# Performance work log

Hardware: AMD Instinct MI355X
Metric: run time of the kernel (lower is better)

## Reference

```python
import jax, jax.numpy as jnp
import numpy as np

B, N, D, H, O = 8, 2048, 64, 64, 64
ALPHA = 2.0  # LeakyReLU negative slope per module default
NEG = -9e15


def _lin(x, W, b):
    # torch nn.Linear: y = x @ W.T + b, W is [out, in]
    return x @ W.T + b


def setup_inputs() -> dict:
    key = jax.random.key(0)
    ks = jax.random.split(key, 32)
    f32 = jnp.float32
    x = jax.random.normal(ks[0], (B, N, D), f32)
    adj = jax.random.randint(ks[1], (B, N, N), 0, 2).astype(f32)
    c = jax.random.normal(ks[2], (B, N, H), f32)
    h = jax.random.normal(ks[3], (B, N, H), f32)
    s = 0.1
    W = jax.random.normal(ks[4], (D, H), f32) * s           # GAT weight
    a = jax.random.normal(ks[5], (2 * H, 1), f32) * s       # GAT attention vector
    def lin(k, out_d, in_d):
        k1, k2 = jax.random.split(k)
        return (jax.random.normal(k1, (out_d, in_d), f32) * s,
                jax.random.normal(k2, (out_d,), f32) * s)
    Wf, bWf = lin(ks[6], H, H); Wi, bWi = lin(ks[7], H, H)
    Wo, bWo = lin(ks[8], H, H); Wc, bWc = lin(ks[9], H, H)
    Uf, bUf = lin(ks[10], H, D); Ui, bUi = lin(ks[11], H, D)
    Uo, bUo = lin(ks[12], H, D); Uc, bUc = lin(ks[13], H, D)
    Wout, bout = lin(ks[14], O, 2 * H)
    return dict(x=x, adj=adj, c=c, h=h, W=W, a=a,
                Wf=Wf, bWf=bWf, Wi=Wi, bWi=bWi, Wo=Wo, bWo=bWo, Wc=Wc, bWc=bWc,
                Uf=Uf, bUf=bUf, Ui=Ui, bUi=bUi, Uo=Uo, bUo=bUo, Uc=Uc, bUc=bUc,
                Wout=Wout, bout=bout)


def reference(x, adj, c, h, W, a,
              Wf, bWf, Wi, bWi, Wo, bWo, Wc, bWc,
              Uf, bUf, Ui, bUi, Uo, bUo, Uc, bUc,
              Wout, bout):
    # ---- GraphAttentionLayer (eval mode: dropout is identity) ----
    Wh = x @ W                                   # [B,N,H]
    # e[b,i,j] = leakyrelu(a[:H].Wh_i + a[H:].Wh_j) -- same math as the
    a_src = (Wh @ a[:H]).squeeze(-1)             # [B,N]
    a_dst = (Wh @ a[H:]).squeeze(-1)             # [B,N]
    e = jax.nn.leaky_relu(a_src[:, :, None] + a_dst[:, None, :], ALPHA)  # [B,N,N]
    att = jnp.where(adj > 0, e, NEG)
    att = jax.nn.softmax(att, axis=2)
    x_hidden = jax.nn.elu(att @ Wh)              # [B,N,H] (concat=True)
    # ---- LSTMLayer step ----
    f_t = jax.nn.sigmoid(_lin(h, Wf, bWf) + _lin(x, Uf, bUf))
    i_t = jax.nn.sigmoid(_lin(h, Wi, bWi) + _lin(x, Ui, bUi))
    o_t = jax.nn.sigmoid(_lin(h, Wo, bWo) + _lin(x, Uo, bUo))
    c_hat = jnp.tanh(_lin(h, Wc, bWc) + _lin(x, Uc, bUc))
    c_t = f_t * c + i_t * c_hat
    h_t = o_t * jax.nn.relu(c_t)                 # gate = nn.ReLU() default
    total = jnp.concatenate([x_hidden, h_t], axis=2)  # [B,N,2H]
    output = jax.nn.relu(_lin(total, Wout, bout))     # [B,N,O]
    return (output, h_t, c_t)
```

## Files before the change

### kernel.cpp

```cpp
#include <hip/hip_runtime.h>
#include <math.h>

#define B_ 8
#define N_ 2048
#define NT_ (B_*N_)
#define OUTSZ (NT_*64)

#define WS_ASRC  0
#define WS_ADST  (WS_ASRC + NT_)
#define WS_EJ    (WS_ADST + NT_)
#define WS_C1    (WS_EJ + NT_)
#define WS_C2    (WS_C1 + NT_)
#define WS_THR   (WS_C2 + NT_)
#define WS_GMAX  (WS_THR + NT_)
#define WS_WT    (WS_GMAX + 32)
#define WS_BB    (WS_WT + 128*256)
#define WS_WOT   (WS_BB + 256)
#define WS_PD    (WS_WOT + 128*64)
#define WS_PN    (WS_PD + 4*NT_)

typedef float f32x4 __attribute__((ext_vector_type(4)));
typedef __bf16 bf16x8 __attribute__((ext_vector_type(8)));
typedef __bf16 bf16x4 __attribute__((ext_vector_type(4)));

__device__ __forceinline__ float lrelu2(float x) { return x > 0.f ? x : 2.f * x; }
__device__ __forceinline__ float f4get(const float4& v, int k) { return k==0?v.x:(k==1?v.y:(k==2?v.z:v.w)); }

__global__ __launch_bounds__(256) void k1_wh(const float* __restrict__ x, const float* __restrict__ W,
                                             const float* __restrict__ a, float* __restrict__ ws,
                                             __bf16* __restrict__ whT,
                                             const float* Wf, const float* Wi, const float* Wo, const float* Wc,
                                             const float* Uf, const float* Ui, const float* Uo, const float* Uc,
                                             const float* bWf, const float* bWi, const float* bWo, const float* bWc,
                                             const float* bUf, const float* bUi, const float* bUo, const float* bUc,
                                             const float* Wout)
{
    __shared__ float xl[64 * 68];
    __shared__ float Wl[64 * 68];
    int t = threadIdx.x;
    if (blockIdx.x >= 256) {
        int idx = (blockIdx.x - 256) * 256 + t;
        if (idx < 128 * 256) {
            int k = idx >> 8, o = idx & 255;
            int g = o >> 6, u = o & 63;
            const float* Wg = (g == 0) ? Wf : (g == 1) ? Wi : (g == 2) ? Wo : Wc;
            const float* Ug = (g == 0) ? Uf : (g == 1) ? Ui : (g == 2) ? Uo : Uc;
            ws[WS_WT + idx] = (k < 64) ? Wg[u * 64 + k] : Ug[u * 64 + (k - 64)];
        } else if (idx < 128 * 256 + 256) {
            int o = idx - 128 * 256;
            int g = o >> 6, u = o & 63;
            const float* bW = (g == 0) ? bWf : (g == 1) ? bWi : (g == 2) ? bWo : bWc;
            const float* bU = (g == 0) ? bUf : (g == 1) ? bUi : (g == 2) ? bUo : bUc;
            ws[WS_BB + o] = bW[u] + bU[u];
        } else if (idx < 128 * 256 + 256 + 128 * 64) {
            int j = idx - (128 * 256 + 256);
            int k = j >> 6, u = j & 63;
            ws[WS_WOT + j] = Wout[u * 128 + k];
        }
        return;
    }
    int i0 = blockIdx.x * 64;
    #pragma unroll
    for (int it = 0; it < 4; ++it) {
        int f = t + 256 * it;
        int r = f >> 4, q = f & 15;
        *(float4*)&xl[r * 68 + q * 4] = *(const float4*)&x[i0 * 64 + f * 4];
        *(float4*)&Wl[r * 68 + q * 4] = *(const float4*)&W[f * 4];
    }
    __syncthreads();
    int cg = t & 15, rg = t >> 4;
    int c0 = cg * 4, r0 = rg * 4;
    float acc[4][4] = {};
    #pragma unroll
    for (int d0 = 0; d0 < 64; d0 += 4) {
        float4 wv[4], xv[4];
        #pragma unroll
        for (int k = 0; k < 4; ++k) wv[k] = *(float4*)&Wl[(d0 + k) * 68 + c0];
        #pragma unroll
        for (int ri = 0; ri < 4; ++ri) xv[ri] = *(float4*)&xl[(r0 + ri) * 68 + d0];
        #pragma unroll
        for (int ri = 0; ri < 4; ++ri)
            #pragma unroll
            for (int k = 0; k < 4; ++k) {
                float xs = f4get(xv[ri], k);
                acc[ri][0] += xs * wv[k].x; acc[ri][1] += xs * wv[k].y;
                acc[ri][2] += xs * wv[k].z; acc[ri][3] += xs * wv[k].w;
            }
    }
    int b = i0 >> 11;
    int rowb0 = (i0 & 2047) + r0;
    #pragma unroll
    for (int cj = 0; cj < 4; ++cj) {
        bf16x4 v;
        v[0] = (__bf16)acc[0][cj]; v[1] = (__bf16)acc[1][cj];
        v[2] = (__bf16)acc[2][cj]; v[3] = (__bf16)acc[3][cj];
        *(bf16x4*)&whT[((size_t)(b * 64 + c0 + cj)) * N_ + rowb0] = v;
    }
    float4 a0 = *(const float4*)&a[c0];
    float4 a1 = *(const float4*)&a[64 + c0];
    #pragma unroll
    for (int ri = 0; ri < 4; ++ri) {
        int row = i0 + r0 + ri;
        float s0 = acc[ri][0]*a0.x + acc[ri][1]*a0.y + acc[ri][2]*a0.z + acc[ri][3]*a0.w;
        float s1 = acc[ri][0]*a1.x + acc[ri][1]*a1.y + acc[ri][2]*a1.z + acc[ri][3]*a1.w;
        #pragma unroll
        for (int m = 1; m < 16; m <<= 1) { s0 += __shfl_xor(s0, m, 64); s1 += __shfl_xor(s1, m, 64); }
        if (cg == 0) { ws[WS_ASRC + row] = s0; ws[WS_ADST + row] = s1; }
    }
}

__global__ __launch_bounds__(256) void k1b_prep(float* ws)
{
    __shared__ float red[256];
    __shared__ float gsh;
    int b = blockIdx.x, t = threadIdx.x;
    float m = -3.0e38f;
    for (int j = t; j < N_; j += 256) {
        float v = ws[WS_ADST + b * N_ + j];
        ws[WS_EJ + b * N_ + j] = __expf(v);
        m = fmaxf(m, v);
    }
    red[t] = m; __syncthreads();
    for (int s = 128; s > 0; s >>= 1) { if (t < s) red[t] = fmaxf(red[t], red[t + s]); __syncthreads(); }
    if (t == 0) { gsh = red[0]; ws[WS_GMAX + b] = red[0]; }
    __syncthreads();
    float gmax = gsh;
    for (int i = t; i < N_; i += 256) {
        float as = ws[WS_ASRC + b * N_ + i];
        float M = lrelu2(as + gmax);
        ws[WS_C1 + b * N_ + i]  = __expf(as - M);
        ws[WS_C2 + b * N_ + i]  = __expf(2.f * as - M);
        ws[WS_THR + b * N_ + i] = __expf(-as);
    }
}

__global__ __launch_bounds__(512, 4) void k2v4(const float* __restrict__ adj,
                                               const __bf16* __restrict__ whT,
                                               float* __restrict__ ws)
{
    __shared__ float lsa[2][8][16][68];
    __shared__ float lsd[2][8][16];
    int tid = threadIdx.x;
    int lane = tid & 63, w = tid >> 6;
    int r = lane & 15, g = lane >> 4;
    int jr = blockIdx.x & 3;
    int rslab = blockIdx.x >> 2;
    int b = rslab >> 4;
    int row_base = rslab * 128;
    int jbeg = jr * 512 + w * 64;

    bf16x8 bfr[2][4];
    #pragma unroll
    for (int ks = 0; ks < 2; ++ks)
        #pragma unroll
        for (int n = 0; n < 4; ++n)
            bfr[ks][n] = *(const bf16x8*)&whT[(size_t)(b * 64 + n * 16 + r) * N_ + jbeg + ks * 32 + g * 8];
    float ejr[2][8];
    #pragma unroll
    for (int ks = 0; ks < 2; ++ks) {
        float4 e0 = *(const float4*)&ws[WS_EJ + b * N_ + jbeg + ks * 32 + g * 8];
        float4 e1 = *(const float4*)&ws[WS_EJ + b * N_ + jbeg + ks * 32 + g * 8 + 4];
        ejr[ks][0]=e0.x; ejr[ks][1]=e0.y; ejr[ks][2]=e0.z; ejr[ks][3]=e0.w;
        ejr[ks][4]=e1.x; ejr[ks][5]=e1.y; ejr[ks][6]=e1.z; ejr[ks][7]=e1.w;
    }

    float4 av[3][4];
    float c1v[3], c2v[3], thv[3];

#define LDT(T, S)                                                                  \
    {                                                                              \
        int row0_ = row_base + (T) * 16;                                           \
        const float* ap_ = &adj[(size_t)(row0_ + r) * N_ + jbeg];                  \
        av[S][0] = *(const float4*)&ap_[g * 8];                                    \
        av[S][1] = *(const float4*)&ap_[g * 8 + 4];                                \
        av[S][2] = *(const float4*)&ap_[32 + g * 8];                               \
        av[S][3] = *(const float4*)&ap_[32 + g * 8 + 4];                           \
        c1v[S] = ws[WS_C1 + row0_ + r];                                            \
        c2v[S] = ws[WS_C2 + row0_ + r];                                            \
        thv[S] = ws[WS_THR + row0_ + r];                                           \
    }

    LDT(0, 0);
    LDT(1, 1);

    #pragma unroll
    for (int t = 0; t < 8; ++t) {
        const int s = t % 3;
        if (t + 2 < 8) { LDT(t + 2, (t + 2) % 3); }
        f32x4 acc[4] = {{0.f,0.f,0.f,0.f},{0.f,0.f,0.f,0.f},{0.f,0.f,0.f,0.f},{0.f,0.f,0.f,0.f}};
        float dsum = 0.f;
        float c1 = c1v[s], c2 = c2v[s], thr = thv[s];
        #pragma unroll
        for (int ks = 0; ks < 2; ++ks) {
            bf16x8 af;
            float ds_ = 0.f;
            #pragma unroll
            for (int e = 0; e < 8; ++e) {
                float avv = f4get(e < 4 ? av[s][ks * 2] : av[s][ks * 2 + 1], e & 3);
                float E = ejr[ks][e];
                float p = (E > thr) ? c1 * E : (c2 * E) * E;
                p = (avv > 0.f) ? p : 0.f;
                ds_ += p;
                af[e] = (__bf16)p;
            }
            dsum += ds_;
            #pragma unroll
            for (int n = 0; n < 4; ++n)
                acc[n] = __builtin_amdgcn_mfma_f32_16x16x32_bf16(af, bfr[ks][n], acc[n], 0, 0, 0);
        }
        dsum += __shfl_xor(dsum, 16, 64);
        dsum += __shfl_xor(dsum, 32, 64);
        #pragma unroll
        for (int n = 0; n < 4; ++n)
            #pragma unroll
            for (int i = 0; i < 4; ++i)
                lsa[t & 1][w][g * 4 + i][n * 16 + r] = acc[n][i];
        if (g == 0) lsd[t & 1][w][r] = dsum;
        asm volatile("s_waitcnt lgkmcnt(0)" ::: "memory");
        __builtin_amdgcn_s_barrier();
        asm volatile("" ::: "memory");
        if (tid < 256) {
            int rl = tid >> 4, h0 = (tid & 15) * 4;
            float4 sv = make_float4(0.f, 0.f, 0.f, 0.f);
            #pragma unroll
            for (int w2 = 0; w2 < 8; ++w2) {
                float4 q = *(const float4*)&lsa[t & 1][w2][rl][h0];
                sv.x += q.x; sv.y += q.y; sv.z += q.z; sv.w += q.w;
            }
            int row0 = row_base + t * 16;
            *(float4*)&ws[WS_PN + ((size_t)jr * NT_ + row0 + rl) * 64 + h0] = sv;
            if (tid < 16) {
                float d = 0.f;
                #pragma unroll
                for (int w2 = 0; w2 < 8; ++w2) d += lsd[t & 1][w2][tid];
                ws[WS_PD + jr * NT_ + row0 + tid] = d;
            }
        }
    }
#undef LDT
}

__global__ __launch_bounds__(256) void k3_lstm(const float* __restrict__ x, const float* __restrict__ c,
                                               const float* __restrict__ h, const float* __restrict__ ws,
                                               float* __restrict__ out)
{
    __shared__ float Al[16 * 132];
    __shared__ float gl[16 * 260];
    int t = threadIdx.x;
    int base = blockIdx.x * 16;
    {
        int r = t >> 4, k0 = (t & 15) * 8;
        const float* src = (k0 < 64) ? &h[(base + r) * 64 + k0] : &x[(base + r) * 64 + (k0 - 64)];
        *(float4*)&Al[r * 132 + k0]     = *(const float4*)&src[0];
        *(float4*)&Al[r * 132 + k0 + 4] = *(const float4*)&src[4];
    }
    __syncthreads();
    int og = t & 63, rg = t >> 6;
    int o0 = og * 4;
    const float* WT = &ws[WS_WT];
    float acc[4][4] = {};
    #pragma unroll
    for (int k0 = 0; k0 < 128; k0 += 4) {
        float4 wv[4], av[4];
        #pragma unroll
        for (int kk = 0; kk < 4; ++kk) wv[kk] = *(const float4*)&WT[(k0 + kk) * 256 + o0];
        #pragma unroll
        for (int rr = 0; rr < 4; ++rr) av[rr] = *(float4*)&Al[(rg + 4 * rr) * 132 + k0];
        #pragma unroll
        for (int rr = 0; rr < 4; ++rr)
            #pragma unroll
            for (int kk = 0; kk < 4; ++kk) {
                float as = f4get(av[rr], kk);
                acc[rr][0] += as * wv[kk].x; acc[rr][1] += as * wv[kk].y;
                acc[rr][2] += as * wv[kk].z; acc[rr][3] += as * wv[kk].w;
            }
    }
    float4 bbv = *(const float4*)&ws[WS_BB + o0];
    #pragma unroll
    for (int rr = 0; rr < 4; ++rr) {
        int r = rg + 4 * rr;
        *(float4*)&gl[r * 260 + o0] = make_float4(acc[rr][0] + bbv.x, acc[rr][1] + bbv.y,
                                                  acc[rr][2] + bbv.z, acc[rr][3] + bbv.w);
    }
    __syncthreads();
    int u = t & 63, rq = t >> 6;
    #pragma unroll
    for (int pp = 0; pp < 4; ++pp) {
        int r = rq + 4 * pp;
        float gf = gl[r * 260 + u];
        float gi = gl[r * 260 + 64 + u];
        float go = gl[r * 260 + 128 + u];
        float gc = gl[r * 260 + 192 + u];
        float fg = 1.f / (1.f + __expf(-gf));
        float ig = 1.f / (1.f + __expf(-gi));
        float oo = 1.f / (1.f + __expf(-go));
        float ch = tanhf(gc);
        float cv = c[(base + r) * 64 + u];
        float ct = fg * cv + ig * ch;
        float ht = oo * fmaxf(ct, 0.f);
        out[OUTSZ + (base + r) * 64 + u] = ht;
        out[2 * OUTSZ + (base + r) * 64 + u] = ct;
    }
}

__global__ __launch_bounds__(256) void k5_out(const float* __restrict__ ws, const float* __restrict__ bout,
                                              float* __restrict__ out)
{
    __shared__ float Al[64 * 132];
    int t = threadIdx.x;
    int base = blockIdx.x * 64;
    const float* ht = &out[OUTSZ];
    #pragma unroll
    for (int it = 0; it < 8; ++it) {
        int f = t + 256 * it;
        int r = f >> 5, q = f & 31;
        int k0 = q * 4;
        int row = base + r;
        float4 v;
        if (k0 < 64) {
            float4 s = make_float4(0.f, 0.f, 0.f, 0.f);
            float d = 0.f;
            #pragma unroll
            for (int jr = 0; jr < 4; ++jr) {
                float4 p = *(const float4*)&ws[WS_PN + ((size_t)jr * NT_ + row) * 64 + k0];
                s.x += p.x; s.y += p.y; s.z += p.z; s.w += p.w;
                d += ws[WS_PD + jr * NT_ + row];
            }
            float inv = 1.f / d;
            v.x = s.x * inv; v.x = v.x > 0.f ? v.x : expm1f(v.x);
            v.y = s.y * inv; v.y = v.y > 0.f ? v.y : expm1f(v.y);
            v.z = s.z * inv; v.z = v.z > 0.f ? v.z : expm1f(v.z);
            v.w = s.w * inv; v.w = v.w > 0.f ? v.w : expm1f(v.w);
        } else {
            v = *(const float4*)&ht[(size_t)row * 64 + (k0 - 64)];
        }
        *(float4*)&Al[r * 132 + k0] = v;
    }
    __syncthreads();
    int cg = t & 15, rgG = t >> 4;
    int c0 = cg * 4, r0 = rgG * 4;
    const float* WT = &ws[WS_WOT];
    float acc[4][4] = {};
    #pragma unroll
    for (int k0 = 0; k0 < 128; k0 += 4) {
        float4 wv[4], av[4];
        #pragma unroll
        for (int kk = 0; kk < 4; ++kk) wv[kk] = *(const float4*)&WT[(k0 + kk) * 64 + c0];
        #pragma unroll
        for (int ri = 0; ri < 4; ++ri) av[ri] = *(float4*)&Al[(r0 + ri) * 132 + k0];
        #pragma unroll
        for (int ri = 0; ri < 4; ++ri)
            #pragma unroll
            for (int kk = 0; kk < 4; ++kk) {
                float as = f4get(av[ri], kk);
                acc[ri][0] += as * wv[kk].x; acc[ri][1] += as * wv[kk].y;
                acc[ri][2] += as * wv[kk].z; acc[ri][3] += as * wv[kk].w;
            }
    }
    float4 bo = *(const float4*)&bout[c0];
    #pragma unroll
    for (int ri = 0; ri < 4; ++ri) {
        int row = base + r0 + ri;
        float4 o;
        o.x = fmaxf(acc[ri][0] + bo.x, 0.f);
        o.y = fmaxf(acc[ri][1] + bo.y, 0.f);
        o.z = fmaxf(acc[ri][2] + bo.z, 0.f);
        o.w = fmaxf(acc[ri][3] + bo.w, 0.f);
        *(float4*)&out[row * 64 + c0] = o;
    }
}

extern "C" void kernel_launch(void* const* d_in, const int* in_sizes, int n_in,
                              void* d_out, int out_size, void* d_ws, size_t ws_size,
                              hipStream_t stream)
{
    const float* x    = (const float*)d_in[0];
    const float* adj  = (const float*)d_in[1];
    const float* c    = (const float*)d_in[2];
    const float* h    = (const float*)d_in[3];
    const float* W    = (const float*)d_in[4];
    const float* a    = (const float*)d_in[5];
    const float* Wf   = (const float*)d_in[6];
    const float* bWf  = (const float*)d_in[7];
    const float* Wi   = (const float*)d_in[8];
    const float* bWi  = (const float*)d_in[9];
    const float* Wo   = (const float*)d_in[10];
    const float* bWo  = (const float*)d_in[11];
    const float* Wc   = (const float*)d_in[12];
    const float* bWc  = (const float*)d_in[13];
    const float* Uf   = (const float*)d_in[14];
    const float* bUf  = (const float*)d_in[15];
    const float* Ui   = (const float*)d_in[16];
    const float* bUi  = (const float*)d_in[17];
    const float* Uo   = (const float*)d_in[18];
    const float* bUo  = (const float*)d_in[19];
    const float* Uc   = (const float*)d_in[20];
    const float* bUc  = (const float*)d_in[21];
    const float* Wout = (const float*)d_in[22];
    const float* bout = (const float*)d_in[23];
    float* out = (float*)d_out;
    float* ws  = (float*)d_ws;
    __bf16* whT = (__bf16*)out;

    k1_wh<<<417, 256, 0, stream>>>(x, W, a, ws, whT,
                                   Wf, Wi, Wo, Wc, Uf, Ui, Uo, Uc,
                                   bWf, bWi, bWo, bWc, bUf, bUi, bUo, bUc, Wout);
    k1b_prep<<<B_, 256, 0, stream>>>(ws);
    k3_lstm<<<NT_ / 16, 256, 0, stream>>>(x, c, h, ws, out);
    k2v4<<<512, 512, 0, stream>>>(adj, whT, ws);
    k5_out<<<NT_ / 64, 256, 0, stream>>>(ws, bout, out);
}
```

Baseline: 106.7 us.

## Fold softmax prep into Wh and attention kernels, split columns eight ways

Removes the separate per-batch prep kernel. The global max of a_dst is now reduced with an order-preserving atomicMax inside k1_wh, and the exp factors (E_j, c1, c2, threshold) are recomputed inline in the attention kernel. The attention kernel moves from 512 to 256 threads with 8 column splits instead of 4. It drops one prefetch stage (double- instead of triple-buffered adj loads), which doubles the partial-sum buffers that k5 must reduce. This trades a serial single-block-per-batch launch and its workspace traffic for extra exp work, atomics, a memset and more partial-sum reads.

```diff
diff --git a/kernel.cpp b/kernel.cpp
--- a/kernel.cpp
+++ b/kernel.cpp
@@ -8,16 +8,12 @@
 
 #define WS_ASRC  0
 #define WS_ADST  (WS_ASRC + NT_)
-#define WS_EJ    (WS_ADST + NT_)
-#define WS_C1    (WS_EJ + NT_)
-#define WS_C2    (WS_C1 + NT_)
-#define WS_THR   (WS_C2 + NT_)
-#define WS_GMAX  (WS_THR + NT_)
+#define WS_GMAX  (WS_ADST + NT_)
 #define WS_WT    (WS_GMAX + 32)
 #define WS_BB    (WS_WT + 128*256)
 #define WS_WOT   (WS_BB + 256)
 #define WS_PD    (WS_WOT + 128*64)
-#define WS_PN    (WS_PD + 4*NT_)
+#define WS_PN    (WS_PD + 8*NT_)
 
 typedef float f32x4 __attribute__((ext_vector_type(4)));
 typedef __bf16 bf16x8 __attribute__((ext_vector_type(8)));
@@ -98,6 +94,7 @@
     }
     float4 a0 = *(const float4*)&a[c0];
     float4 a1 = *(const float4*)&a[64 + c0];
+    float wmax = -3.0e38f;
     #pragma unroll
     for (int ri = 0; ri < 4; ++ri) {
         int row = i0 + r0 + ri;
@@ -106,48 +103,34 @@
         #pragma unroll
         for (int m = 1; m < 16; m <<= 1) { s0 += __shfl_xor(s0, m, 64); s1 += __shfl_xor(s1, m, 64); }
         if (cg == 0) { ws[WS_ASRC + row] = s0; ws[WS_ADST + row] = s1; }
-    }
-}
-
-__global__ __launch_bounds__(256) void k1b_prep(float* ws)
-{
-    __shared__ float red[256];
-    __shared__ float gsh;
-    int b = blockIdx.x, t = threadIdx.x;
-    float m = -3.0e38f;
-    for (int j = t; j < N_; j += 256) {
-        float v = ws[WS_ADST + b * N_ + j];
-        ws[WS_EJ + b * N_ + j] = __expf(v);
-        m = fmaxf(m, v);
-    }
-    red[t] = m; __syncthreads();
-    for (int s = 128; s > 0; s >>= 1) { if (t < s) red[t] = fmaxf(red[t], red[t + s]); __syncthreads(); }
-    if (t == 0) { gsh = red[0]; ws[WS_GMAX + b] = red[0]; }
-    __syncthreads();
-    float gmax = gsh;
-    for (int i = t; i < N_; i += 256) {
-        float as = ws[WS_ASRC + b * N_ + i];
-        float M = lrelu2(as + gmax);
-        ws[WS_C1 + b * N_ + i]  = __expf(as - M);
-        ws[WS_C2 + b * N_ + i]  = __expf(2.f * as - M);
-        ws[WS_THR + b * N_ + i] = __expf(-as);
-    }
-}
-
-__global__ __launch_bounds__(512, 4) void k2v4(const float* __restrict__ adj,
-                                               const __bf16* __restrict__ whT,
-                                               float* __restrict__ ws)
-{
-    __shared__ float lsa[2][8][16][68];
-    __shared__ float lsd[2][8][16];
+        float m16 = fmaxf(s1, __shfl_xor(s1, 16, 64));
+        m16 = fmaxf(m16, __shfl_xor(m16, 32, 64));
+        wmax = fmaxf(wmax, m16);
+    }
+    if ((t & 63) == 0) {
+        unsigned u = __float_as_uint(wmax);
+        unsigned e = (u & 0x80000000u) ? ~u : (u | 0x80000000u);
+        atomicMax(((unsigned*)&ws[WS_GMAX]) + b, e);
+    }
+}
+
+__global__ __launch_bounds__(256) void k2v5(const float* __restrict__ adj,
+                                            const __bf16* __restrict__ whT,
+                                            float* __restrict__ ws)
+{
+    __shared__ float lsa[2][4][16][68];
+    __shared__ float lsd[2][4][16];
     int tid = threadIdx.x;
     int lane = tid & 63, w = tid >> 6;
     int r = lane & 15, g = lane >> 4;
-    int jr = blockIdx.x & 3;
-    int rslab = blockIdx.x >> 2;
+    int jr = blockIdx.x & 7;
+    int rslab = blockIdx.x >> 3;
     int b = rslab >> 4;
     int row_base = rslab * 128;
-    int jbeg = jr * 512 + w * 64;
+    int jbeg = jr * 256 + w * 64;
+
+    unsigned ge = ((const unsigned*)&ws[WS_GMAX])[b];
+    float gmax = (ge & 0x80000000u) ? __uint_as_float(ge & 0x7FFFFFFFu) : __uint_as_float(~ge);
 
     bf16x8 bfr[2][4];
     #pragma unroll
@@ -158,14 +141,14 @@
     float ejr[2][8];
     #pragma unroll
     for (int ks = 0; ks < 2; ++ks) {
-        float4 e0 = *(const float4*)&ws[WS_EJ + b * N_ + jbeg + ks * 32 + g * 8];
-        float4 e1 = *(const float4*)&ws[WS_EJ + b * N_ + jbeg + ks * 32 + g * 8 + 4];
-        ejr[ks][0]=e0.x; ejr[ks][1]=e0.y; ejr[ks][2]=e0.z; ejr[ks][3]=e0.w;
-        ejr[ks][4]=e1.x; ejr[ks][5]=e1.y; ejr[ks][6]=e1.z; ejr[ks][7]=e1.w;
-    }
-
-    float4 av[3][4];
-    float c1v[3], c2v[3], thv[3];
+        float4 d0 = *(const float4*)&ws[WS_ADST + b * N_ + jbeg + ks * 32 + g * 8];
+        float4 d1 = *(const float4*)&ws[WS_ADST + b * N_ + jbeg + ks * 32 + g * 8 + 4];
+        ejr[ks][0]=__expf(d0.x); ejr[ks][1]=__expf(d0.y); ejr[ks][2]=__expf(d0.z); ejr[ks][3]=__expf(d0.w);
+        ejr[ks][4]=__expf(d1.x); ejr[ks][5]=__expf(d1.y); ejr[ks][6]=__expf(d1.z); ejr[ks][7]=__expf(d1.w);
+    }
+
+    float4 av[2][4];
+    float asv[2];
 
 #define LDT(T, S)                                                                  \
     {                                                                              \
@@ -175,21 +158,22 @@
         av[S][1] = *(const float4*)&ap_[g * 8 + 4];                                \
         av[S][2] = *(const float4*)&ap_[32 + g * 8];                               \
         av[S][3] = *(const float4*)&ap_[32 + g * 8 + 4];                           \
-        c1v[S] = ws[WS_C1 + row0_ + r];                                            \
-        c2v[S] = ws[WS_C2 + row0_ + r];                                            \
-        thv[S] = ws[WS_THR + row0_ + r];                                           \
+        asv[S] = ws[WS_ASRC + row0_ + r];                                          \
     }
 
     LDT(0, 0);
-    LDT(1, 1);
 
     #pragma unroll
     for (int t = 0; t < 8; ++t) {
-        const int s = t % 3;
-        if (t + 2 < 8) { LDT(t + 2, (t + 2) % 3); }
+        const int s = t & 1;
+        if (t + 1 < 8) { LDT(t + 1, (t + 1) & 1); }
+        float as = asv[s];
+        float M  = lrelu2(as + gmax);
+        float c1 = __expf(as - M);
+        float c2 = __expf(2.f * as - M);
+        float thr = __expf(-as);
         f32x4 acc[4] = {{0.f,0.f,0.f,0.f},{0.f,0.f,0.f,0.f},{0.f,0.f,0.f,0.f},{0.f,0.f,0.f,0.f}};
         float dsum = 0.f;
-        float c1 = c1v[s], c2 = c2v[s], thr = thv[s];
         #pragma unroll
         for (int ks = 0; ks < 2; ++ks) {
             bf16x8 af;
@@ -214,27 +198,24 @@
         for (int n = 0; n < 4; ++n)
             #pragma unroll
             for (int i = 0; i < 4; ++i)
-                lsa[t & 1][w][g * 4 + i][n * 16 + r] = acc[n][i];
-        if (g == 0) lsd[t & 1][w][r] = dsum;
+                lsa[s][w][g * 4 + i][n * 16 + r] = acc[n][i];
+        if (g == 0) lsd[s][w][r] = dsum;
         asm volatile("s_waitcnt lgkmcnt(0)" ::: "memory");
         __builtin_amdgcn_s_barrier();
         asm volatile("" ::: "memory");
-        if (tid < 256) {
+        {
             int rl = tid >> 4, h0 = (tid & 15) * 4;
             float4 sv = make_float4(0.f, 0.f, 0.f, 0.f);
             #pragma unroll
-            for (int w2 = 0; w2 < 8; ++w2) {
-                float4 q = *(const float4*)&lsa[t & 1][w2][rl][h0];
+            for (int w2 = 0; w2 < 4; ++w2) {
+                float4 q = *(const float4*)&lsa[s][w2][rl][h0];
                 sv.x += q.x; sv.y += q.y; sv.z += q.z; sv.w += q.w;
             }
             int row0 = row_base + t * 16;
             *(float4*)&ws[WS_PN + ((size_t)jr * NT_ + row0 + rl) * 64 + h0] = sv;
-            if (tid < 16) {
-                float d = 0.f;
-                #pragma unroll
-                for (int w2 = 0; w2 < 8; ++w2) d += lsd[t & 1][w2][tid];
-                ws[WS_PD + jr * NT_ + row0 + tid] = d;
-            }
+            if (tid < 16)
+                ws[WS_PD + jr * NT_ + row0 + tid] =
+                    lsd[s][0][tid] + lsd[s][1][tid] + lsd[s][2][tid] + lsd[s][3][tid];
         }
     }
 #undef LDT
@@ -321,7 +302,7 @@
             float4 s = make_float4(0.f, 0.f, 0.f, 0.f);
             float d = 0.f;
             #pragma unroll
-            for (int jr = 0; jr < 4; ++jr) {
+            for (int jr = 0; jr < 8; ++jr) {
                 float4 p = *(const float4*)&ws[WS_PN + ((size_t)jr * NT_ + row) * 64 + k0];
                 s.x += p.x; s.y += p.y; s.z += p.z; s.w += p.w;
                 d += ws[WS_PD + jr * NT_ + row];
@@ -402,11 +383,12 @@
     float* ws  = (float*)d_ws;
     __bf16* whT = (__bf16*)out;
 
+    hipMemsetAsync((void*)(ws + WS_GMAX), 0, 32 * sizeof(float), stream);
+
     k1_wh<<<417, 256, 0, stream>>>(x, W, a, ws, whT,
                                    Wf, Wi, Wo, Wc, Uf, Ui, Uo, Uc,
                                    bWf, bWi, bWo, bWc, bUf, bUi, bUo, bUc, Wout);
-    k1b_prep<<<B_, 256, 0, stream>>>(ws);
     k3_lstm<<<NT_ / 16, 256, 0, stream>>>(x, c, h, ws, out);
-    k2v4<<<512, 512, 0, stream>>>(adj, whT, ws);
+    k2v5<<<1024, 256, 0, stream>>>(adj, whT, ws);
     k5_out<<<NT_ / 64, 256, 0, stream>>>(ws, bout, out);
 }
```

Measured after the change: 102.7 us. 3.8% less time.
